# Kernel optimization log

Measured on AMD Instinct MI355X. Metric: run time of the kernel, lower is better.

The kernel has to match this reference:

```python
import jax, jax.numpy as jnp
import numpy as np

BS, L, IMG, RS = 512, 68, 224, 7
R2 = RS * RS
DEPTH_SCALE = 500.0
VALID_RANGE = 90.0
THR = 1e-4


def setup_inputs() -> dict:
    key = jax.random.key(0)
    k1, k2, k3 = jax.random.split(key, 3)
    rel_depth_pred = jax.random.normal(k1, (BS, L, L), dtype=jnp.float32)
    depth = jax.random.uniform(k2, (BS, 1, IMG, IMG), dtype=jnp.float32)
    # landmarks in pixel coords well inside the 224px image so regions are valid
    landmarks = jax.random.uniform(k3, (BS, L, 2), dtype=jnp.float32) * 180.0 + 22.0
    scale_factor = jnp.ones((BS, 2), dtype=jnp.float32)
    bbox = jnp.zeros((BS, 4), dtype=jnp.float32)
    return {"rel_depth_pred": rel_depth_pred, "depth": depth,
            "landmarks": landmarks, "scale_factor": scale_factor, "bbox": bbox}


def _extract_landmark_depth(depth, landmarks, scale_factor, bbox):
    bs, img = depth.shape[0], depth.shape[3]
    # normalized landmark coords in [-1, 1]
    face_lm = (landmarks - bbox[:, None, :2]) * scale_factor[:, None, :] / img * 2.0 - 1.0  # [bs,L,2]
    x = jnp.linspace(-RS / 2.0, RS / 2.0, RS) / img * 2.0
    A, B = jnp.meshgrid(x, x, indexing='ij')          # A[i,j]=x[i], B[i,j]=x[j]
    offsets = jnp.stack([B, A], axis=2)               # torch: stack(meshgrid([x,x])[::-1], dim=2)
    grid = face_lm[:, :, None, None, :] + offsets     # [bs,L,RS,RS,2]
    grid = grid.reshape(bs, L * R2, 2)
    # F.grid_sample mode='nearest', padding='zeros', align_corners=False
    ix = ((grid[..., 0] + 1.0) * img - 1.0) * 0.5
    iy = ((grid[..., 1] + 1.0) * img - 1.0) * 0.5
    xi = jnp.round(ix).astype(jnp.int32)
    yi = jnp.round(iy).astype(jnp.int32)
    valid = (xi >= 0) & (xi < img) & (yi >= 0) & (yi < img)
    xi = jnp.clip(xi, 0, img - 1)
    yi = jnp.clip(yi, 0, img - 1)
    flat = depth.reshape(bs, img * img)
    vals = jnp.take_along_axis(flat, yi * img + xi, axis=1) * valid.astype(depth.dtype)
    regions = vals.reshape(bs, L, R2)
    s = jnp.sort(regions, axis=2)                     # ascending per landmark region
    m = s > THR
    m = m.at[:, :, 0].set(False)                      # torch zeroes index 0 before the diff
    trans = m[:, :, 1:] & ~m[:, :, :-1]               # single 0->1 transition (m is monotone)
    has = jnp.any(trans, axis=2)
    st = jnp.where(has, jnp.argmax(trans, axis=2) + 1, R2 - 1)  # fallback: last index
    med_ind = (st + R2 - 1) // 2                      # ((st + 48)/2).long()
    median = jnp.take_along_axis(s, med_ind[..., None], axis=2)[..., 0]  # [bs,L]
    # torch.median over dim=1: lower median = (L-1)//2-th order statistic
    med_of_med = jnp.sort(median, axis=1)[:, (L - 1) // 2]
    median_mask = jnp.abs(median - med_of_med[:, None]) < VALID_RANGE / DEPTH_SCALE
    return median, median_mask


def reference(rel_depth_pred, depth, landmarks, scale_factor, bbox):
    median, median_mask = _extract_landmark_depth(depth, landmarks, scale_factor, bbox)
    median = median * DEPTH_SCALE
    median_diff = median[:, :, None] - median[:, None, :]            # [bs,L,L]
    fm = median_mask.astype(rel_depth_pred.dtype)
    median_rel_mask = fm[:, :, None] * fm[:, None, :]                # [bs,L,L]
    d = rel_depth_pred - median_diff
    ad = jnp.abs(d)
    loss_ele = jnp.where(ad < 1.0, 0.5 * d * d, ad - 0.5)            # smooth_l1, reduction='none'
    loss = jnp.sum(loss_ele * median_rel_mask) / (jnp.sum(median_rel_mask) + 1e-4)
    return loss, median_diff, median_rel_mask
```

## Files before the change

### kernel.cpp

```cpp
#include <hip/hip_runtime.h>
#include <cfloat>
#include <math.h>

static constexpr int kBS  = 512;
static constexpr int kL   = 68;
static constexpr int kIMG = 224;
static constexpr int kR2  = 49;
static constexpr int kLL  = kL * kL;
static constexpr int kPairsTotal = kBS * kLL / 2;
static constexpr int kOutBlocks = kPairsTotal / 256;

__device__ __forceinline__ float lin_off(int k) {
  float step = __fdiv_rn((float)k, 6.0f);
  float a = __fmul_rn(-3.5f, __fsub_rn(1.0f, step));
  float b = __fmul_rn(3.5f, step);
  float x = __fadd_rn(a, b);
  return __fmul_rn(__fdiv_rn(x, 224.0f), 2.0f);
}

__global__ __launch_bounds__(256) void k_median(
    const float* __restrict__ depth, const float* __restrict__ lmk,
    const float* __restrict__ scale, const float* __restrict__ bbox,
    float* __restrict__ med) {
  int wave = blockIdx.x * 4 + (threadIdx.x >> 6);
  int lane = threadIdx.x & 63;
  if (wave >= kBS * kL) return;
  int b = wave / kL;

  float lmx = lmk[wave * 2 + 0];
  float lmy = lmk[wave * 2 + 1];
  float sx = scale[b * 2 + 0], sy = scale[b * 2 + 1];
  float bx = bbox[b * 4 + 0],  by = bbox[b * 4 + 1];

  float tx = __fsub_rn(lmx, bx);
  tx = __fmul_rn(tx, sx); tx = __fdiv_rn(tx, 224.0f); tx = __fmul_rn(tx, 2.0f);
  float flmx = __fsub_rn(tx, 1.0f);
  float ty = __fsub_rn(lmy, by);
  ty = __fmul_rn(ty, sy); ty = __fdiv_rn(ty, 224.0f); ty = __fmul_rn(ty, 2.0f);
  float flmy = __fsub_rn(ty, 1.0f);

  float v = INFINITY;
  if (lane < kR2) {
    int i = lane / 7, j = lane - i * 7;
    float gx = __fadd_rn(flmx, lin_off(j));
    float gy = __fadd_rn(flmy, lin_off(i));
    float ix = __fmul_rn(__fsub_rn(__fmul_rn(__fadd_rn(gx, 1.0f), 224.0f), 1.0f), 0.5f);
    float iy = __fmul_rn(__fsub_rn(__fmul_rn(__fadd_rn(gy, 1.0f), 224.0f), 1.0f), 0.5f);
    int xi = (int)rintf(ix), yi = (int)rintf(iy);
    bool valid = (xi >= 0) && (xi < kIMG) && (yi >= 0) && (yi < kIMG);
    int xc = min(max(xi, 0), kIMG - 1), yc = min(max(yi, 0), kIMG - 1);
    float dv = depth[(size_t)b * (kIMG * kIMG) + yc * kIMG + xc];
    v = valid ? dv : 0.0f;
  }

  unsigned long long mle = __ballot(lane < kR2 && v <= 1e-4f);
  int cnt = __popcll(mle);

#pragma unroll
  for (int k = 2; k <= 64; k <<= 1) {
#pragma unroll
    for (int j = k >> 1; j > 0; j >>= 1) {
      float w = __shfl_xor(v, j, 64);
      bool up = ((lane & k) == 0);
      bool lower = ((lane & j) == 0);
      v = (up == lower) ? fminf(v, w) : fmaxf(v, w);
    }
  }

  int st = min(max(cnt, 1), kR2 - 1);
  int kk = (st + kR2 - 1) >> 1;
  float m = __shfl(v, kk, 64);
  if (lane == 0) med[wave] = m;
}

__global__ __launch_bounds__(128) void k_mask(
    const float* __restrict__ med, float2* __restrict__ mf) {
  __shared__ float s[kL];
  __shared__ float mom_s;
  int b = blockIdx.x, t = threadIdx.x;
  if (t < kL) s[t] = med[b * kL + t];
  __syncthreads();
  if (t < kL) {
    float v = s[t];
    int rank = 0;
    for (int j = 0; j < kL; ++j) {
      float vj = s[j];
      rank += ((vj < v) || (vj == v && j < t)) ? 1 : 0;
    }
    if (rank == (kL - 1) / 2) mom_s = v;
  }
  __syncthreads();
  if (t < kL) {
    float v = s[t];
    float diff = fabsf(__fsub_rn(v, mom_s));
    float2 o;
    o.x = __fmul_rn(v, 500.0f);
    o.y = (diff < 0.18f) ? 1.0f : 0.0f;
    mf[b * kL + t] = o;
  }
}

__global__ __launch_bounds__(256) void k_out(
    const float* __restrict__ rdp, const float2* __restrict__ mf,
    float* __restrict__ out_diff, float* __restrict__ out_mask,
    double* __restrict__ part) {
  __shared__ double sn[4], sd[4];
  int t = blockIdx.x * 256 + threadIdx.x;
  int e = t * 2;
  unsigned b = (unsigned)e / (unsigned)kLL;
  int r = e - (int)b * kLL;
  unsigned i0 = (unsigned)r / (unsigned)kL;
  int j0 = r - (int)i0 * kL;
  unsigned i1 = (j0 == kL - 1) ? i0 + 1 : i0;
  int j1 = (j0 == kL - 1) ? 0 : j0 + 1;

  const float2* mfb = mf + b * kL;
  float2 a0 = mfb[i0], a1 = mfb[i1];
  float2 c0 = mfb[j0], c1 = mfb[j1];
  float2 rp = ((const float2*)rdp)[t];

  float diff0 = __fsub_rn(a0.x, c0.x);
  float diff1 = __fsub_rn(a1.x, c1.x);
  float mv0 = __fmul_rn(a0.y, c0.y);
  float mv1 = __fmul_rn(a1.y, c1.y);
  out_diff[e] = diff0; out_diff[e + 1] = diff1;
  out_mask[e] = mv0;   out_mask[e + 1] = mv1;

  float d0 = __fsub_rn(rp.x, diff0), d1 = __fsub_rn(rp.y, diff1);
  float ad0 = fabsf(d0), ad1 = fabsf(d1);
  float le0 = (ad0 < 1.0f) ? __fmul_rn(__fmul_rn(0.5f, d0), d0) : __fsub_rn(ad0, 0.5f);
  float le1 = (ad1 < 1.0f) ? __fmul_rn(__fmul_rn(0.5f, d1), d1) : __fsub_rn(ad1, 0.5f);
  double pn = (double)__fmul_rn(le0, mv0) + (double)__fmul_rn(le1, mv1);
  double pd = (double)mv0 + (double)mv1;

  for (int off = 32; off > 0; off >>= 1) {
    pn += __shfl_down(pn, off, 64);
    pd += __shfl_down(pd, off, 64);
  }
  int w = threadIdx.x >> 6;
  if ((threadIdx.x & 63) == 0) { sn[w] = pn; sd[w] = pd; }
  __syncthreads();
  if (threadIdx.x == 0) {
    part[2 * blockIdx.x + 0] = sn[0] + sn[1] + sn[2] + sn[3];
    part[2 * blockIdx.x + 1] = sd[0] + sd[1] + sd[2] + sd[3];
  }
}

__global__ __launch_bounds__(256) void k_final(
    const double* __restrict__ part, float* __restrict__ out0) {
  __shared__ double sn[4], sd[4];
  double pn = 0.0, pd = 0.0;
  for (int i = threadIdx.x; i < kOutBlocks; i += 256) {
    pn += part[2 * i + 0];
    pd += part[2 * i + 1];
  }
  for (int off = 32; off > 0; off >>= 1) {
    pn += __shfl_down(pn, off, 64);
    pd += __shfl_down(pd, off, 64);
  }
  int w = threadIdx.x >> 6;
  if ((threadIdx.x & 63) == 0) { sn[w] = pn; sd[w] = pd; }
  __syncthreads();
  if (threadIdx.x == 0) {
    double tn = sn[0] + sn[1] + sn[2] + sn[3];
    double td = sd[0] + sd[1] + sd[2] + sd[3];
    out0[0] = (float)(tn / (td + 1e-4));
  }
}

extern "C" void kernel_launch(void* const* d_in, const int* in_sizes, int n_in,
                              void* d_out, int out_size, void* d_ws, size_t ws_size,
                              hipStream_t stream) {
  const float* rdp   = (const float*)d_in[0];
  const float* depth = (const float*)d_in[1];
  const float* lmk   = (const float*)d_in[2];
  const float* scale = (const float*)d_in[3];
  const float* bbox  = (const float*)d_in[4];

  float* out = (float*)d_out;
  float* out_diff = out + 1;
  float* out_mask = out + 1 + (size_t)kBS * kLL;

  char* ws = (char*)d_ws;
  float*  med  = (float*)(ws);
  float2* mf   = (float2*)(ws + 139264);
  double* part = (double*)(ws + 139264 + 278528);

  int nWaves = kBS * kL;
  int nBlk1 = (nWaves + 3) / 4;
  k_median<<<dim3(nBlk1), dim3(256), 0, stream>>>(depth, lmk, scale, bbox, med);
  k_mask<<<dim3(kBS), dim3(128), 0, stream>>>(med, mf);
  k_out<<<dim3(kOutBlocks), dim3(256), 0, stream>>>(rdp, mf, out_diff, out_mask, part);
  k_final<<<dim3(1), dim3(256), 0, stream>>>(part, out);
}
```

Before: 178.4 us.

## Fuse median mask computation into output kernel with per-batch 2D grid

Removes the separate k_mask kernel and its intermediate float2 buffer. The output kernel now runs on a (chunk, batch) grid: each block loads the 68 medians of its batch into shared memory, recomputes the median-of-medians and the mask there, then processes 1024 pairwise elements with one float4 load of rel_depth_pred per thread. This saves a kernel launch and the global round trip through the mf buffer. In exchange, the rank computation is repeated in each of the 5 chunk blocks of a batch, and the last chunk is partly idle.

```diff
diff --git a/kernel.cpp b/kernel.cpp
--- a/kernel.cpp
+++ b/kernel.cpp
@@ -7,8 +7,8 @@
 static constexpr int kIMG = 224;
 static constexpr int kR2  = 49;
 static constexpr int kLL  = kL * kL;
-static constexpr int kPairsTotal = kBS * kLL / 2;
-static constexpr int kOutBlocks = kPairsTotal / 256;
+static constexpr int kChunks = 5;
+static constexpr int kOutBlocks = kBS * kChunks;
 
 __device__ __forceinline__ float lin_off(int k) {
   float step = __fdiv_rn((float)k, 6.0f);
@@ -73,76 +73,70 @@
   if (lane == 0) med[wave] = m;
 }
 
-__global__ __launch_bounds__(128) void k_mask(
-    const float* __restrict__ med, float2* __restrict__ mf) {
-  __shared__ float s[kL];
+__global__ __launch_bounds__(256) void k_out(
+    const float* __restrict__ rdp, const float* __restrict__ med,
+    float* __restrict__ out_diff, float* __restrict__ out_mask,
+    double* __restrict__ part) {
+  __shared__ float s_med[kL], s_m[kL], s_f[kL];
   __shared__ float mom_s;
-  int b = blockIdx.x, t = threadIdx.x;
-  if (t < kL) s[t] = med[b * kL + t];
+  __shared__ double sn[4], sd[4];
+  int b = blockIdx.y, chunk = blockIdx.x, t = threadIdx.x;
+
+  if (t < kL) s_med[t] = med[b * kL + t];
   __syncthreads();
   if (t < kL) {
-    float v = s[t];
+    float v = s_med[t];
     int rank = 0;
     for (int j = 0; j < kL; ++j) {
-      float vj = s[j];
+      float vj = s_med[j];
       rank += ((vj < v) || (vj == v && j < t)) ? 1 : 0;
     }
     if (rank == (kL - 1) / 2) mom_s = v;
   }
   __syncthreads();
   if (t < kL) {
-    float v = s[t];
-    float diff = fabsf(__fsub_rn(v, mom_s));
-    float2 o;
-    o.x = __fmul_rn(v, 500.0f);
-    o.y = (diff < 0.18f) ? 1.0f : 0.0f;
-    mf[b * kL + t] = o;
+    float v = s_med[t];
+    s_m[t] = __fmul_rn(v, 500.0f);
+    s_f[t] = (fabsf(__fsub_rn(v, mom_s)) < 0.18f) ? 1.0f : 0.0f;
   }
-}
+  __syncthreads();
 
-__global__ __launch_bounds__(256) void k_out(
-    const float* __restrict__ rdp, const float2* __restrict__ mf,
-    float* __restrict__ out_diff, float* __restrict__ out_mask,
-    double* __restrict__ part) {
-  __shared__ double sn[4], sd[4];
-  int t = blockIdx.x * 256 + threadIdx.x;
-  int e = t * 2;
-  unsigned b = (unsigned)e / (unsigned)kLL;
-  int r = e - (int)b * kLL;
-  unsigned i0 = (unsigned)r / (unsigned)kL;
-  int j0 = r - (int)i0 * kL;
-  unsigned i1 = (j0 == kL - 1) ? i0 + 1 : i0;
-  int j1 = (j0 == kL - 1) ? 0 : j0 + 1;
-
-  const float2* mfb = mf + b * kL;
-  float2 a0 = mfb[i0], a1 = mfb[i1];
-  float2 c0 = mfb[j0], c1 = mfb[j1];
-  float2 rp = ((const float2*)rdp)[t];
-
-  float diff0 = __fsub_rn(a0.x, c0.x);
-  float diff1 = __fsub_rn(a1.x, c1.x);
-  float mv0 = __fmul_rn(a0.y, c0.y);
-  float mv1 = __fmul_rn(a1.y, c1.y);
-  out_diff[e] = diff0; out_diff[e + 1] = diff1;
-  out_mask[e] = mv0;   out_mask[e + 1] = mv1;
-
-  float d0 = __fsub_rn(rp.x, diff0), d1 = __fsub_rn(rp.y, diff1);
-  float ad0 = fabsf(d0), ad1 = fabsf(d1);
-  float le0 = (ad0 < 1.0f) ? __fmul_rn(__fmul_rn(0.5f, d0), d0) : __fsub_rn(ad0, 0.5f);
-  float le1 = (ad1 < 1.0f) ? __fmul_rn(__fmul_rn(0.5f, d1), d1) : __fsub_rn(ad1, 0.5f);
-  double pn = (double)__fmul_rn(le0, mv0) + (double)__fmul_rn(le1, mv1);
-  double pd = (double)mv0 + (double)mv1;
+  int e = chunk * 1024 + t * 4;
+  double pn = 0.0, pd = 0.0;
+  if (e < kLL) {
+    unsigned i = (unsigned)e / (unsigned)kL;
+    int j = e - (int)i * kL;
+    size_t base = (size_t)b * kLL + e;
+    float4 rp = *(const float4*)(rdp + base);
+    float mi = s_m[i], fi = s_f[i];
+    float rq[4] = {rp.x, rp.y, rp.z, rp.w};
+#pragma unroll
+    for (int q = 0; q < 4; ++q) {
+      float mj = s_m[j + q], fj = s_f[j + q];
+      float diff = __fsub_rn(mi, mj);
+      float mv = __fmul_rn(fi, fj);
+      out_diff[base + q] = diff;
+      out_mask[base + q] = mv;
+      float d = __fsub_rn(rq[q], diff);
+      float ad = fabsf(d);
+      float le = (ad < 1.0f) ? __fmul_rn(__fmul_rn(0.5f, d), d)
+                             : __fsub_rn(ad, 0.5f);
+      pn += (double)__fmul_rn(le, mv);
+      pd += (double)mv;
+    }
+  }
 
   for (int off = 32; off > 0; off >>= 1) {
     pn += __shfl_down(pn, off, 64);
     pd += __shfl_down(pd, off, 64);
   }
-  int w = threadIdx.x >> 6;
-  if ((threadIdx.x & 63) == 0) { sn[w] = pn; sd[w] = pd; }
+  int w = t >> 6;
+  if ((t & 63) == 0) { sn[w] = pn; sd[w] = pd; }
   __syncthreads();
-  if (threadIdx.x == 0) {
-    part[2 * blockIdx.x + 0] = sn[0] + sn[1] + sn[2] + sn[3];
-    part[2 * blockIdx.x + 1] = sd[0] + sd[1] + sd[2] + sd[3];
+  if (t == 0) {
+    int blkid = b * kChunks + chunk;
+    part[2 * blkid + 0] = sn[0] + sn[1] + sn[2] + sn[3];
+    part[2 * blkid + 1] = sd[0] + sd[1] + sd[2] + sd[3];
   }
 }
 
@@ -183,13 +177,11 @@
 
   char* ws = (char*)d_ws;
   float*  med  = (float*)(ws);
-  float2* mf   = (float2*)(ws + 139264);
-  double* part = (double*)(ws + 139264 + 278528);
+  double* part = (double*)(ws + 139264);
 
   int nWaves = kBS * kL;
   int nBlk1 = (nWaves + 3) / 4;
   k_median<<<dim3(nBlk1), dim3(256), 0, stream>>>(depth, lmk, scale, bbox, med);
-  k_mask<<<dim3(kBS), dim3(128), 0, stream>>>(med, mf);
-  k_out<<<dim3(kOutBlocks), dim3(256), 0, stream>>>(rdp, mf, out_diff, out_mask, part);
+  k_out<<<dim3(kChunks, kBS), dim3(256), 0, stream>>>(rdp, med, out_diff, out_mask, part);
   k_final<<<dim3(1), dim3(256), 0, stream>>>(part, out);
 }
```

Measured after the change: 171.5 us. -3.8%, faster.
